# Kernel optimization log

Measured on AMD Instinct MI355X. Metric: run time of the kernel, lower is better.

Reference implementation:

```python
import jax, jax.numpy as jnp
import numpy as np

B, T, I, H, CODE = 256, 512, 1, 1024, 3


def _gru_cell(x, h, Wih, Whh, bih, bhh):
    # x: [B, I], h: [B, H]; torch nn.GRU gate math
    gi = x @ Wih.T + bih            # [B, 3H]
    gh = h @ Whh.T + bhh            # [B, 3H]
    i_r, i_z, i_n = jnp.split(gi, 3, axis=-1)
    h_r, h_z, h_n = jnp.split(gh, 3, axis=-1)
    r = jax.nn.sigmoid(i_r + h_r)
    z = jax.nn.sigmoid(i_z + h_z)
    n = jnp.tanh(i_n + r * h_n)
    return (1.0 - z) * n + z * h


def setup_inputs() -> dict:
    key = jax.random.key(0)
    ks = jax.random.split(key, 16)
    s_i = 1.0 / np.sqrt(H)
    u = lambda k, shape, s: jax.random.uniform(k, shape, jnp.float32, -s, s)
    inp = {
        "input": jax.random.normal(ks[0], (B, T, I), jnp.float32),
        "hidden_state": jnp.zeros((B, H), jnp.float32),
        # encoder GRU
        "Wih_e": u(ks[1], (3 * H, I), s_i), "Whh_e": u(ks[2], (3 * H, H), s_i),
        "bih_e": u(ks[3], (3 * H,), s_i), "bhh_e": u(ks[4], (3 * H,), s_i),
        # linear_enc: H -> 3
        "Wenc": u(ks[5], (CODE, H), s_i), "benc": u(ks[6], (CODE,), s_i),
        # linear_dec: 3 -> H
        "Wdec": u(ks[7], (H, CODE), 1.0 / np.sqrt(CODE)), "bdec": u(ks[8], (H,), 1.0 / np.sqrt(CODE)),
        # decoder GRU
        "Wih_d": u(ks[9], (3 * H, I), s_i), "Whh_d": u(ks[10], (3 * H, H), s_i),
        "bih_d": u(ks[11], (3 * H,), s_i), "bhh_d": u(ks[12], (3 * H,), s_i),
        # linear_out: H -> I
        "Wout": u(ks[13], (I, H), s_i), "bout": u(ks[14], (I,), s_i),
    }
    return inp


def reference(input, hidden_state, Wih_e, Whh_e, bih_e, bhh_e,
              Wenc, benc, Wdec, bdec, Wih_d, Whh_d, bih_d, bhh_d, Wout, bout):
    # ---- Encoder: GRU over the sequence, keep final hidden state ----
    xs = jnp.swapaxes(input, 0, 1)  # [T, B, I]

    def enc_step(h, x_t):
        h = _gru_cell(x_t, h, Wih_e, Whh_e, bih_e, bhh_e)
        return h, None

    h_T, _ = jax.lax.scan(enc_step, hidden_state, xs)
    # bottleneck: linear H->3 + sigmoid (use_linear, use_activation)
    features = jax.nn.sigmoid(h_T @ Wenc.T + benc)  # [B, 3]

    h0 = features @ Wdec.T + bdec                   # [B, H]
    x0 = jnp.zeros((input.shape[0], I), input.dtype)

    def dec_step(carry, _):
        x, h = carry
        h = _gru_cell(x, h, Wih_d, Whh_d, bih_d, bhh_d)
        x = h @ Wout.T + bout                       # [B, I]
        return (x, h), x

    _, ys = jax.lax.scan(dec_step, (x0, h0), None, length=T)  # [T, B, I]
    output = jnp.swapaxes(ys, 0, 1)                 # [B, T, I]

    # ---- Masked MSE (mask is all ones in the source -> plain mean) ----
    loss = jnp.mean((input - output) ** 2)
    return loss, features, output
```

## Files before the change

### kernel.cpp

```cpp
#include <hip/hip_runtime.h>
#include <math.h>

#define B 256
#define T 512
#define H 1024
#define CODE 3
#define NBLK 256

typedef _Float16 f16x8 __attribute__((ext_vector_type(8)));
typedef float f32x4 __attribute__((ext_vector_type(4)));

__device__ __forceinline__ float sigmoidf_(float x) { return 1.0f / (1.0f + __expf(-x)); }
__device__ __forceinline__ float tanhf_(float x) {
    float ax = fabsf(x);
    float t = __expf(-2.0f * ax);
    float r = (1.0f - t) / (1.0f + t);
    return x < 0.f ? -r : r;
}

__device__ __forceinline__ void store_f16_coh(_Float16* p, float v) {
    unsigned u = (unsigned)__builtin_bit_cast(unsigned short, (_Float16)v);
    asm volatile("global_store_short %0, %1, off sc0 sc1" :: "v"(p), "v"(u) : "memory");
}
__device__ __forceinline__ uint4 load_b16_coh(const void* p) {
    uint4 v;
    asm volatile("global_load_dwordx4 %0, %1, off sc0 sc1" : "=v"(v) : "v"(p));
    return v;
}
__device__ __forceinline__ void storef_coh(float* p, float v) {
    __hip_atomic_store(p, v, __ATOMIC_RELAXED, __HIP_MEMORY_SCOPE_AGENT);
}
__device__ __forceinline__ float loadf_coh(const float* p) {
    return __hip_atomic_load((float*)p, __ATOMIC_RELAXED, __HIP_MEMORY_SCOPE_AGENT);
}

__device__ __forceinline__ void bt_barrier(unsigned* flags, int bt, int jt,
                                           unsigned g, int tid) {
    asm volatile("s_waitcnt vmcnt(0)" ::: "memory");
    __syncthreads();
    if (tid == 0)
        __hip_atomic_store(&flags[(bt * 16 + jt) * 32], g,
                           __ATOMIC_RELAXED, __HIP_MEMORY_SCOPE_AGENT);
    if (tid < 16) {
        while (__hip_atomic_load(&flags[(bt * 16 + tid) * 32],
                                 __ATOMIC_RELAXED, __HIP_MEMORY_SCOPE_AGENT) < g)
            __builtin_amdgcn_s_sleep(1);
    }
    __syncthreads();
}

__device__ __forceinline__ void load_weights(f16x8 (&wB)[48], const float* __restrict__ W,
                                             int j, int kh, int kg) {
#pragma unroll
    for (int g = 0; g < 3; ++g)
#pragma unroll
        for (int i = 0; i < 16; ++i) {
            const float* p = W + (((size_t)g << 10) + j) * 1024 + (kh << 9) + (i << 5) + (kg << 3);
            float4 u = *(const float4*)p;
            float4 v = *(const float4*)(p + 4);
            f16x8 o;
            o[0] = (_Float16)u.x; o[1] = (_Float16)u.y; o[2] = (_Float16)u.z; o[3] = (_Float16)u.w;
            o[4] = (_Float16)v.x; o[5] = (_Float16)v.y; o[6] = (_Float16)v.z; o[7] = (_Float16)v.w;
            wB[g * 16 + i] = o;
        }
}

template <bool DEC>
__device__ __forceinline__ void phase(
    int b0, int bt, int jt, int j, int np, int kh, int kg, int r16, int tid, int lane,
    const f16x8 (&wB)[48], float (&hreg)[4],
    _Float16* __restrict__ h16A, _Float16* __restrict__ h16B,
    const float* __restrict__ Wih, const float* __restrict__ bih,
    const float* __restrict__ bhh,
    const float* __restrict__ input, const float* __restrict__ Wout, float bout_v,
    float* __restrict__ xpart, float* __restrict__ outp,
    unsigned* flags, unsigned& g,
    char* Als, f32x4 (*red)[3][64], float* xv_s, float (*xnp)[16])
{
    const float wi_r = Wih[j], wi_z = Wih[1024 + j], wi_n = Wih[2048 + j];
    const float bi_r = bih[j], bi_z = bih[1024 + j], bi_n = bih[2048 + j];
    const float bh_r = bhh[j], bh_z = bhh[1024 + j], bh_n = bhh[2048 + j];
    const float wo = DEC ? Wout[j] : 0.f;
    const int kc = tid & 127;
    const int rb = tid >> 7;

    for (int t = 0; t < T; ++t) {
        const _Float16* hp = (t & 1) ? h16B : h16A;
        _Float16* hn = (t & 1) ? h16A : h16B;

        if (DEC) {
            if (tid < 16) {
                float s = 0.f;
                if (t > 0) {
                    const float* xp = xpart + ((t - 1) & 1) * 4096 + (size_t)(b0 + tid) * 16;
#pragma unroll
                    for (int q = 0; q < 16; ++q) s += loadf_coh(xp + q);
                    s += bout_v;
                    if (jt == 0) outp[(size_t)(b0 + tid) * T + (t - 1)] = s;
                }
                xv_s[tid] = s;
            }
        }

        uint4 tmp[4];
#pragma unroll
        for (int i = 0; i < 4; ++i) {
            int row = i * 4 + rb;
            tmp[i] = load_b16_coh(hp + (((size_t)(b0 + row)) << 10) + (kc << 3));
        }
        asm volatile("s_waitcnt vmcnt(0)" ::: "memory");
#pragma unroll
        for (int i = 0; i < 4; ++i) {
            int row = i * 4 + rb;
            *(uint4*)(Als + row * 2048 + ((kc << 4) ^ ((row & 7) << 4))) = tmp[i];
        }
        __syncthreads();

        f32x4 aR = {0.f, 0.f, 0.f, 0.f}, aZ = {0.f, 0.f, 0.f, 0.f}, aN = {0.f, 0.f, 0.f, 0.f};
#pragma unroll
        for (int i = 0; i < 16; ++i) {
            int kb = (kh << 10) + (i << 6) + (kg << 4);
            f16x8 a = *(const f16x8*)(Als + (r16 << 11) + (kb ^ ((r16 & 7) << 4)));
            aR = __builtin_amdgcn_mfma_f32_16x16x32_f16(a, wB[i], aR, 0, 0, 0);
            aZ = __builtin_amdgcn_mfma_f32_16x16x32_f16(a, wB[16 + i], aZ, 0, 0, 0);
            aN = __builtin_amdgcn_mfma_f32_16x16x32_f16(a, wB[32 + i], aN, 0, 0, 0);
        }

        if (kh == 1) {
            red[np][0][lane] = aR; red[np][1][lane] = aZ; red[np][2][lane] = aN;
        }
        __syncthreads();

        if (kh == 0) {
            f32x4 rR = red[np][0][lane], rZ = red[np][1][lane], rN = red[np][2][lane];
            float xw[4];
#pragma unroll
            for (int reg = 0; reg < 4; ++reg) {
                int brow = kg * 4 + reg;
                int b = b0 + brow;
                float xv = DEC ? xv_s[brow] : input[(size_t)b * T + t];
                float r = sigmoidf_(xv * wi_r + bi_r + aR[reg] + rR[reg] + bh_r);
                float z = sigmoidf_(xv * wi_z + bi_z + aZ[reg] + rZ[reg] + bh_z);
                float n = tanhf_(xv * wi_n + bi_n + r * (aN[reg] + rN[reg] + bh_n));
                float hNew = (1.f - z) * n + z * hreg[reg];
                hreg[reg] = hNew;
                store_f16_coh(hn + ((size_t)b << 10) + j, hNew);
                xw[reg] = hNew * wo;
            }
            if (DEC) {
#pragma unroll
                for (int reg = 0; reg < 4; ++reg) {
                    float v = xw[reg];
                    v += __shfl_xor(v, 1); v += __shfl_xor(v, 2);
                    v += __shfl_xor(v, 4); v += __shfl_xor(v, 8);
                    if (r16 == 0) xnp[np][kg * 4 + reg] = v;
                }
            }
        }
        if (DEC) {
            __syncthreads();
            if (tid < 16) {
                float s = xnp[0][tid] + xnp[1][tid] + xnp[2][tid] + xnp[3][tid];
                storef_coh(xpart + (t & 1) * 4096 + (size_t)(b0 + tid) * 16 + jt, s);
            }
        }
        bt_barrier(flags, bt, jt, ++g, tid);
    }
}

__global__ __launch_bounds__(512, 2) void gru_persistent(
    const float* __restrict__ input, const float* __restrict__ h_init,
    const float* __restrict__ Wih_e, const float* __restrict__ Whh_e,
    const float* __restrict__ bih_e, const float* __restrict__ bhh_e,
    const float* __restrict__ Wenc, const float* __restrict__ benc,
    const float* __restrict__ Wdec, const float* __restrict__ bdec,
    const float* __restrict__ Wih_d, const float* __restrict__ Whh_d,
    const float* __restrict__ bih_d, const float* __restrict__ bhh_d,
    const float* __restrict__ Wout, const float* __restrict__ boutp,
    float* __restrict__ featOut, float* __restrict__ outp,
    _Float16* __restrict__ h16A, _Float16* __restrict__ h16B,
    float* __restrict__ xpart, float* __restrict__ fpart,
    unsigned* flags)
{
    __shared__ __align__(16) char Als[32768];
    __shared__ f32x4 red[4][3][64];
    __shared__ float xv_s[16];
    __shared__ float xnp[4][16];
    __shared__ float fp_np[4][16][3];
    __shared__ float feats[16][3];

    const int tid = threadIdx.x;
    const int lane = tid & 63;
    const int w = tid >> 6;
    const int kh = w & 1;
    const int np = w >> 1;
    const int kg = lane >> 4;
    const int r16 = lane & 15;
    const int bid = blockIdx.x;
    const int bt = bid & 15, jt = bid >> 4;
    const int b0 = bt * 16, j0 = jt * 64;
    const int j = j0 + np * 16 + r16;
    const float bout_v = boutp[0];
    unsigned g = 0;

    f16x8 wB[48];
    float hreg[4] = {0.f, 0.f, 0.f, 0.f};

    if (kh == 0) {
#pragma unroll
        for (int reg = 0; reg < 4; ++reg) {
            int b = b0 + kg * 4 + reg;
            float v = h_init[((size_t)b << 10) + j];
            hreg[reg] = v;
            store_f16_coh(h16A + ((size_t)b << 10) + j, v);
        }
    }
    load_weights(wB, Whh_e, j, kh, kg);
    bt_barrier(flags, bt, jt, ++g, tid);

    phase<false>(b0, bt, jt, j, np, kh, kg, r16, tid, lane, wB, hreg, h16A, h16B,
                 Wih_e, bih_e, bhh_e, input, Wout, bout_v, xpart, outp,
                 flags, g, Als, red, xv_s, xnp);

    {
        float we0 = Wenc[j], we1 = Wenc[1024 + j], we2 = Wenc[2048 + j];
        if (kh == 0) {
#pragma unroll
            for (int reg = 0; reg < 4; ++reg) {
                float h = hreg[reg];
                float p0 = h * we0, p1 = h * we1, p2 = h * we2;
#pragma unroll
                for (int m = 1; m < 16; m <<= 1) {
                    p0 += __shfl_xor(p0, m);
                    p1 += __shfl_xor(p1, m);
                    p2 += __shfl_xor(p2, m);
                }
                if (r16 == 0) {
                    fp_np[np][kg * 4 + reg][0] = p0;
                    fp_np[np][kg * 4 + reg][1] = p1;
                    fp_np[np][kg * 4 + reg][2] = p2;
                }
            }
        }
        __syncthreads();
        if (tid < 48) {
            int bi = tid / 3, c = tid % 3;
            float s = fp_np[0][bi][c] + fp_np[1][bi][c] + fp_np[2][bi][c] + fp_np[3][bi][c];
            storef_coh(fpart + (size_t)(b0 + bi) * 48 + jt * 3 + c, s);
        }
        bt_barrier(flags, bt, jt, ++g, tid);

        if (tid < 48) {
            int bi = tid / 3, c = tid % 3;
            float s = 0.f;
            const float* fp = fpart + (size_t)(b0 + bi) * 48 + c;
#pragma unroll
            for (int q = 0; q < 16; ++q) s += loadf_coh(fp + q * 3);
            float f = sigmoidf_(s + benc[c]);
            feats[bi][c] = f;
            if (jt == 0) featOut[(b0 + bi) * 3 + c] = f;
        }
        __syncthreads();

        if (kh == 0) {
#pragma unroll
            for (int reg = 0; reg < 4; ++reg) {
                int brow = kg * 4 + reg;
                int b = b0 + brow;
                float v = feats[brow][0] * Wdec[j * 3 + 0] + feats[brow][1] * Wdec[j * 3 + 1] +
                          feats[brow][2] * Wdec[j * 3 + 2] + bdec[j];
                hreg[reg] = v;
                store_f16_coh(h16A + ((size_t)b << 10) + j, v);
            }
        }
        load_weights(wB, Whh_d, j, kh, kg);
        bt_barrier(flags, bt, jt, ++g, tid);
    }

    phase<true>(b0, bt, jt, j, np, kh, kg, r16, tid, lane, wB, hreg, h16A, h16B,
                Wih_d, bih_d, bhh_d, input, Wout, bout_v, xpart, outp,
                flags, g, Als, red, xv_s, xnp);

    if (jt == 0 && tid < 16) {
        const float* xp = xpart + 4096 + (size_t)(b0 + tid) * 16;
        float s = 0.f;
#pragma unroll
        for (int q = 0; q < 16; ++q) s += loadf_coh(xp + q);
        outp[(size_t)(b0 + tid) * T + (T - 1)] = s + bout_v;
    }
}

__global__ __launch_bounds__(256) void loss_partial(
    const float* __restrict__ input, const float* __restrict__ outp,
    float* __restrict__ partial)
{
    int idx = blockIdx.x * blockDim.x + threadIdx.x;
    float s = 0.f;
    for (int i = idx; i < B * T; i += gridDim.x * blockDim.x) {
        float d = input[i] - outp[i];
        s += d * d;
    }
#pragma unroll
    for (int off = 32; off; off >>= 1) s += __shfl_down(s, off);
    __shared__ float ws[4];
    if ((threadIdx.x & 63) == 0) ws[threadIdx.x >> 6] = s;
    __syncthreads();
    if (threadIdx.x == 0) partial[blockIdx.x] = ws[0] + ws[1] + ws[2] + ws[3];
}

__global__ __launch_bounds__(256) void loss_final(
    const float* __restrict__ partial, float* __restrict__ loss)
{
    int tid = threadIdx.x;
    float s = partial[tid];
#pragma unroll
    for (int off = 32; off; off >>= 1) s += __shfl_down(s, off);
    __shared__ float ws[4];
    if ((tid & 63) == 0) ws[tid >> 6] = s;
    __syncthreads();
    if (tid == 0) loss[0] = (ws[0] + ws[1] + ws[2] + ws[3]) * (1.0f / (float)(B * T));
}

extern "C" void kernel_launch(void* const* d_in, const int* in_sizes, int n_in,
                              void* d_out, int out_size, void* d_ws, size_t ws_size,
                              hipStream_t stream) {
    const float* input = (const float*)d_in[0];
    const float* h_init = (const float*)d_in[1];
    const float* Wih_e = (const float*)d_in[2];
    const float* Whh_e = (const float*)d_in[3];
    const float* bih_e = (const float*)d_in[4];
    const float* bhh_e = (const float*)d_in[5];
    const float* Wenc  = (const float*)d_in[6];
    const float* benc  = (const float*)d_in[7];
    const float* Wdec  = (const float*)d_in[8];
    const float* bdec  = (const float*)d_in[9];
    const float* Wih_d = (const float*)d_in[10];
    const float* Whh_d = (const float*)d_in[11];
    const float* bih_d = (const float*)d_in[12];
    const float* bhh_d = (const float*)d_in[13];
    const float* Wout  = (const float*)d_in[14];
    const float* bout  = (const float*)d_in[15];
    (void)in_sizes; (void)n_in; (void)out_size; (void)ws_size;

    float* out = (float*)d_out;
    float* lossp = out;
    float* feat = out + 1;
    float* outp = out + 1 + B * CODE;

    char* ws = (char*)d_ws;
    _Float16* h16A = (_Float16*)ws;                  ws += (size_t)B * H * 2;
    _Float16* h16B = (_Float16*)ws;                  ws += (size_t)B * H * 2;
    float* xpart = (float*)ws;                       ws += 2 * 4096 * 4;
    float* fpart = (float*)ws;                       ws += (size_t)B * 48 * 4;
    float* partial = (float*)ws;                     ws += 256 * 4;
    unsigned* flags = (unsigned*)ws;                 ws += 16 * 16 * 32 * 4;

    hipMemsetAsync(flags, 0, 16 * 16 * 32 * 4, stream);

    gru_persistent<<<dim3(NBLK), dim3(512), 0, stream>>>(
        input, h_init, Wih_e, Whh_e, bih_e, bhh_e, Wenc, benc, Wdec, bdec,
        Wih_d, Whh_d, bih_d, bhh_d, Wout, bout,
        feat, outp, h16A, h16B, xpart, fpart, flags);

    loss_partial<<<256, 256, 0, stream>>>(input, outp, partial);
    loss_final<<<1, 256, 0, stream>>>(partial, lossp);
}
```

Baseline: 6.513 ms.

## Split batch tile into two half-groups with separate flags and fuse decoder output projection

Each 16-row batch tile is now processed as two 8-row halves, each with its own flag group. A block can start on one half while the other half's producers are still finishing, so inter-block synchronisation overlaps with compute. The hidden state is stored in a blocked layout so each half-tile is read contiguously. The decoder output x = h·Wout is no longer built from per-block partial sums in a separate exchange buffer; each block recomputes it directly from the shared h tile using Wout held in registers. This removes a synchronisation round per step, at the cost of two waits per step, redundant MFMA work on half-empty tiles, and extra register use.

```diff
diff --git a/kernel.cpp b/kernel.cpp
--- a/kernel.cpp
+++ b/kernel.cpp
@@ -4,7 +4,6 @@
 #define B 256
 #define T 512
 #define H 1024
-#define CODE 3
 #define NBLK 256
 
 typedef _Float16 f16x8 __attribute__((ext_vector_type(8)));
@@ -34,19 +33,18 @@
     return __hip_atomic_load((float*)p, __ATOMIC_RELAXED, __HIP_MEMORY_SCOPE_AGENT);
 }
 
-__device__ __forceinline__ void bt_barrier(unsigned* flags, int bt, int jt,
-                                           unsigned g, int tid) {
+__device__ __forceinline__ void wait_group(unsigned* fl, unsigned g, int tid) {
+    if (tid < 16) {
+        while (__hip_atomic_load(&fl[tid * 32], __ATOMIC_RELAXED, __HIP_MEMORY_SCOPE_AGENT) < g)
+            __builtin_amdgcn_s_sleep(1);
+    }
+    __syncthreads();
+}
+__device__ __forceinline__ void signal_group(unsigned* fl, int jt, unsigned g, int tid) {
     asm volatile("s_waitcnt vmcnt(0)" ::: "memory");
     __syncthreads();
     if (tid == 0)
-        __hip_atomic_store(&flags[(bt * 16 + jt) * 32], g,
-                           __ATOMIC_RELAXED, __HIP_MEMORY_SCOPE_AGENT);
-    if (tid < 16) {
-        while (__hip_atomic_load(&flags[(bt * 16 + tid) * 32],
-                                 __ATOMIC_RELAXED, __HIP_MEMORY_SCOPE_AGENT) < g)
-            __builtin_amdgcn_s_sleep(1);
-    }
-    __syncthreads();
+        __hip_atomic_store(&fl[jt * 32], g, __ATOMIC_RELAXED, __HIP_MEMORY_SCOPE_AGENT);
 }
 
 __device__ __forceinline__ void load_weights(f16x8 (&wB)[48], const float* __restrict__ W,
@@ -66,105 +64,95 @@
 }
 
 template <bool DEC>
-__device__ __forceinline__ void phase(
+__device__ __forceinline__ void run_phase(
     int b0, int bt, int jt, int j, int np, int kh, int kg, int r16, int tid, int lane,
-    const f16x8 (&wB)[48], float (&hreg)[4],
-    _Float16* __restrict__ h16A, _Float16* __restrict__ h16B,
+    int wv, int ridx,
+    const f16x8 (&wB)[48], float (&hreg)[4], const float (&wout_r)[16],
+    _Float16* __restrict__ hx,
     const float* __restrict__ Wih, const float* __restrict__ bih,
     const float* __restrict__ bhh,
-    const float* __restrict__ input, const float* __restrict__ Wout, float bout_v,
-    float* __restrict__ xpart, float* __restrict__ outp,
-    unsigned* flags, unsigned& g,
-    char* Als, f32x4 (*red)[3][64], float* xv_s, float (*xnp)[16])
+    const float* __restrict__ input, float bout_v, float* __restrict__ outp,
+    unsigned* fl0, unsigned* fl1, unsigned& g0, unsigned& g1,
+    char* Als, f32x4 (*red)[3][72], float* xv_s)
 {
-    const float wi_r = Wih[j], wi_z = Wih[1024 + j], wi_n = Wih[2048 + j];
-    const float bi_r = bih[j], bi_z = bih[1024 + j], bi_n = bih[2048 + j];
-    const float bh_r = bhh[j], bh_z = bhh[1024 + j], bh_n = bhh[2048 + j];
-    const float wo = DEC ? Wout[j] : 0.f;
-    const int kc = tid & 127;
-    const int rb = tid >> 7;
+    const float wi_r = Wih[j], wi_z = Wih[H + j], wi_n = Wih[2 * H + j];
+    const float bi_r = bih[j], bi_z = bih[H + j], bi_n = bih[2 * H + j];
+    const float bh_r = bhh[j], bh_z = bhh[H + j], bh_n = bhh[2 * H + j];
+    const int p0 = tid >> 6, w8 = tid & 63;
+    const int srl = w8 >> 3, scc = w8 & 7;
 
     for (int t = 0; t < T; ++t) {
-        const _Float16* hp = (t & 1) ? h16B : h16A;
-        _Float16* hn = (t & 1) ? h16A : h16B;
-
-        if (DEC) {
-            if (tid < 16) {
-                float s = 0.f;
-                if (t > 0) {
-                    const float* xp = xpart + ((t - 1) & 1) * 4096 + (size_t)(b0 + tid) * 16;
-#pragma unroll
-                    for (int q = 0; q < 16; ++q) s += loadf_coh(xp + q);
-                    s += bout_v;
-                    if (jt == 0) outp[(size_t)(b0 + tid) * T + (t - 1)] = s;
+        const int par_r = t & 1, par_w = (t + 1) & 1;
+#pragma unroll
+        for (int s = 0; s < 2; ++s) {
+            unsigned& g = s ? g1 : g0;
+            unsigned* fl = s ? fl1 : fl0;
+            wait_group(fl, g, tid);
+
+            const _Float16* src = hx + ((size_t)(par_r * 2 + s) * 256 + bt * 16) * 512;
+            uint4 v0 = load_b16_coh(src + (size_t)p0 * 512 + w8 * 8);
+            uint4 v1 = load_b16_coh(src + (size_t)(p0 + 8) * 512 + w8 * 8);
+            asm volatile("s_waitcnt vmcnt(0)" ::: "memory");
+            {
+                int row = s * 8 + srl;
+                int xo = (row & 7) << 4;
+                *(uint4*)(Als + row * 2048 + ((((p0) * 8 + scc) * 16) ^ xo)) = v0;
+                *(uint4*)(Als + row * 2048 + ((((p0 + 8) * 8 + scc) * 16) ^ xo)) = v1;
+            }
+            __syncthreads();
+
+            if (DEC) {
+                int arow = s * 8 + wv;
+                const char* ab = Als + arow * 2048;
+                int xo = wv << 4;
+                f16x8 a0 = *(const f16x8*)(ab + ((lane * 32) ^ xo));
+                f16x8 a1 = *(const f16x8*)(ab + (((lane * 32) + 16) ^ xo));
+                float sum = 0.f;
+#pragma unroll
+                for (int i = 0; i < 8; ++i)
+                    sum += (float)a0[i] * wout_r[i] + (float)a1[i] * wout_r[8 + i];
+#pragma unroll
+                for (int m = 1; m < 64; m <<= 1) sum += __shfl_xor(sum, m);
+                if (lane == 0) {
+                    float xv = (t > 0) ? (sum + bout_v) : 0.f;
+                    xv_s[s * 8 + wv] = xv;
+                    if (t > 0 && (jt >> 3) == s && (jt & 7) == wv)
+                        outp[(size_t)(b0 + s * 8 + wv) * T + (t - 1)] = xv;
                 }
-                xv_s[tid] = s;
-            }
-        }
-
-        uint4 tmp[4];
-#pragma unroll
-        for (int i = 0; i < 4; ++i) {
-            int row = i * 4 + rb;
-            tmp[i] = load_b16_coh(hp + (((size_t)(b0 + row)) << 10) + (kc << 3));
-        }
-        asm volatile("s_waitcnt vmcnt(0)" ::: "memory");
-#pragma unroll
-        for (int i = 0; i < 4; ++i) {
-            int row = i * 4 + rb;
-            *(uint4*)(Als + row * 2048 + ((kc << 4) ^ ((row & 7) << 4))) = tmp[i];
-        }
-        __syncthreads();
-
-        f32x4 aR = {0.f, 0.f, 0.f, 0.f}, aZ = {0.f, 0.f, 0.f, 0.f}, aN = {0.f, 0.f, 0.f, 0.f};
-#pragma unroll
-        for (int i = 0; i < 16; ++i) {
-            int kb = (kh << 10) + (i << 6) + (kg << 4);
-            f16x8 a = *(const f16x8*)(Als + (r16 << 11) + (kb ^ ((r16 & 7) << 4)));
-            aR = __builtin_amdgcn_mfma_f32_16x16x32_f16(a, wB[i], aR, 0, 0, 0);
-            aZ = __builtin_amdgcn_mfma_f32_16x16x32_f16(a, wB[16 + i], aZ, 0, 0, 0);
-            aN = __builtin_amdgcn_mfma_f32_16x16x32_f16(a, wB[32 + i], aN, 0, 0, 0);
-        }
-
-        if (kh == 1) {
-            red[np][0][lane] = aR; red[np][1][lane] = aZ; red[np][2][lane] = aN;
-        }
-        __syncthreads();
-
-        if (kh == 0) {
-            f32x4 rR = red[np][0][lane], rZ = red[np][1][lane], rN = red[np][2][lane];
-            float xw[4];
-#pragma unroll
-            for (int reg = 0; reg < 4; ++reg) {
-                int brow = kg * 4 + reg;
-                int b = b0 + brow;
-                float xv = DEC ? xv_s[brow] : input[(size_t)b * T + t];
-                float r = sigmoidf_(xv * wi_r + bi_r + aR[reg] + rR[reg] + bh_r);
-                float z = sigmoidf_(xv * wi_z + bi_z + aZ[reg] + rZ[reg] + bh_z);
-                float n = tanhf_(xv * wi_n + bi_n + r * (aN[reg] + rN[reg] + bh_n));
-                float hNew = (1.f - z) * n + z * hreg[reg];
-                hreg[reg] = hNew;
-                store_f16_coh(hn + ((size_t)b << 10) + j, hNew);
-                xw[reg] = hNew * wo;
-            }
-            if (DEC) {
+            }
+
+            f32x4 aR = {0.f, 0.f, 0.f, 0.f}, aZ = {0.f, 0.f, 0.f, 0.f}, aN = {0.f, 0.f, 0.f, 0.f};
+#pragma unroll
+            for (int i = 0; i < 16; ++i) {
+                int kb = (kh << 10) + (i << 6) + (kg << 4);
+                f16x8 a = *(const f16x8*)(Als + (r16 << 11) + (kb ^ ((r16 & 7) << 4)));
+                aR = __builtin_amdgcn_mfma_f32_16x16x32_f16(a, wB[i], aR, 0, 0, 0);
+                aZ = __builtin_amdgcn_mfma_f32_16x16x32_f16(a, wB[16 + i], aZ, 0, 0, 0);
+                aN = __builtin_amdgcn_mfma_f32_16x16x32_f16(a, wB[32 + i], aN, 0, 0, 0);
+            }
+            if (kh == 1) {
+                red[np][0][ridx] = aR; red[np][1][ridx] = aZ; red[np][2][ridx] = aN;
+            }
+            __syncthreads();
+
+            if (kh == 0 && (kg >> 1) == s) {
+                f32x4 rR = red[np][0][ridx], rZ = red[np][1][ridx], rN = red[np][2][ridx];
+                _Float16* dst = hx + ((size_t)(par_w * 2 + s) * 256 + bt * 16 + jt) * 512;
 #pragma unroll
                 for (int reg = 0; reg < 4; ++reg) {
-                    float v = xw[reg];
-                    v += __shfl_xor(v, 1); v += __shfl_xor(v, 2);
-                    v += __shfl_xor(v, 4); v += __shfl_xor(v, 8);
-                    if (r16 == 0) xnp[np][kg * 4 + reg] = v;
+                    int row = kg * 4 + reg;
+                    int b = b0 + row;
+                    float xv = DEC ? xv_s[row] : input[(size_t)b * T + t];
+                    float r = sigmoidf_(xv * wi_r + bi_r + aR[reg] + rR[reg] + bh_r);
+                    float z = sigmoidf_(xv * wi_z + bi_z + aZ[reg] + rZ[reg] + bh_z);
+                    float n = tanhf_(xv * wi_n + bi_n + r * (aN[reg] + rN[reg] + bh_n));
+                    float hNew = (1.f - z) * n + z * hreg[reg];
+                    hreg[reg] = hNew;
+                    store_f16_coh(dst + (row - s * 8) * 64 + np * 16 + r16, hNew);
                 }
             }
-        }
-        if (DEC) {
-            __syncthreads();
-            if (tid < 16) {
-                float s = xnp[0][tid] + xnp[1][tid] + xnp[2][tid] + xnp[3][tid];
-                storef_coh(xpart + (t & 1) * 4096 + (size_t)(b0 + tid) * 16 + jt, s);
-            }
-        }
-        bt_barrier(flags, bt, jt, ++g, tid);
+            signal_group(fl, jt, ++g, tid);
+        }
     }
 }
 
@@ -178,67 +166,73 @@
     const float* __restrict__ bih_d, const float* __restrict__ bhh_d,
     const float* __restrict__ Wout, const float* __restrict__ boutp,
     float* __restrict__ featOut, float* __restrict__ outp,
-    _Float16* __restrict__ h16A, _Float16* __restrict__ h16B,
-    float* __restrict__ xpart, float* __restrict__ fpart,
+    _Float16* __restrict__ hx, float* __restrict__ fpart,
     unsigned* flags)
 {
     __shared__ __align__(16) char Als[32768];
-    __shared__ f32x4 red[4][3][64];
+    __shared__ f32x4 red[4][3][72];
     __shared__ float xv_s[16];
-    __shared__ float xnp[4][16];
     __shared__ float fp_np[4][16][3];
     __shared__ float feats[16][3];
 
     const int tid = threadIdx.x;
     const int lane = tid & 63;
-    const int w = tid >> 6;
-    const int kh = w & 1;
-    const int np = w >> 1;
+    const int wv = tid >> 6;
+    const int kh = wv & 1;
+    const int np = wv >> 1;
     const int kg = lane >> 4;
     const int r16 = lane & 15;
+    const int ridx = lane + (lane >> 3);
     const int bid = blockIdx.x;
     const int bt = bid & 15, jt = bid >> 4;
     const int b0 = bt * 16, j0 = jt * 64;
     const int j = j0 + np * 16 + r16;
     const float bout_v = boutp[0];
-    unsigned g = 0;
+    unsigned* fl0 = flags + bt * 512;
+    unsigned* fl1 = flags + 8192 + bt * 512;
+    unsigned g0 = 0, g1 = 0;
 
     f16x8 wB[48];
     float hreg[4] = {0.f, 0.f, 0.f, 0.f};
+    float wout_r[16] = {};
 
     if (kh == 0) {
 #pragma unroll
         for (int reg = 0; reg < 4; ++reg) {
-            int b = b0 + kg * 4 + reg;
+            int row = kg * 4 + reg;
+            int b = b0 + row;
             float v = h_init[((size_t)b << 10) + j];
             hreg[reg] = v;
-            store_f16_coh(h16A + ((size_t)b << 10) + j, v);
+            int s = kg >> 1;
+            _Float16* dst = hx + ((size_t)(0 * 2 + s) * 256 + bt * 16 + jt) * 512;
+            store_f16_coh(dst + (row - s * 8) * 64 + np * 16 + r16, v);
         }
     }
     load_weights(wB, Whh_e, j, kh, kg);
-    bt_barrier(flags, bt, jt, ++g, tid);
-
-    phase<false>(b0, bt, jt, j, np, kh, kg, r16, tid, lane, wB, hreg, h16A, h16B,
-                 Wih_e, bih_e, bhh_e, input, Wout, bout_v, xpart, outp,
-                 flags, g, Als, red, xv_s, xnp);
+    signal_group(fl0, jt, ++g0, tid);
+    signal_group(fl1, jt, ++g1, tid);
+
+    run_phase<false>(b0, bt, jt, j, np, kh, kg, r16, tid, lane, wv, ridx,
+                     wB, hreg, wout_r, hx, Wih_e, bih_e, bhh_e,
+                     input, bout_v, outp, fl0, fl1, g0, g1, Als, red, xv_s);
 
     {
-        float we0 = Wenc[j], we1 = Wenc[1024 + j], we2 = Wenc[2048 + j];
+        float we0 = Wenc[j], we1 = Wenc[H + j], we2 = Wenc[2 * H + j];
         if (kh == 0) {
 #pragma unroll
             for (int reg = 0; reg < 4; ++reg) {
                 float h = hreg[reg];
-                float p0 = h * we0, p1 = h * we1, p2 = h * we2;
+                float q0 = h * we0, q1 = h * we1, q2 = h * we2;
 #pragma unroll
                 for (int m = 1; m < 16; m <<= 1) {
-                    p0 += __shfl_xor(p0, m);
-                    p1 += __shfl_xor(p1, m);
-                    p2 += __shfl_xor(p2, m);
+                    q0 += __shfl_xor(q0, m);
+                    q1 += __shfl_xor(q1, m);
+                    q2 += __shfl_xor(q2, m);
                 }
                 if (r16 == 0) {
-                    fp_np[np][kg * 4 + reg][0] = p0;
-                    fp_np[np][kg * 4 + reg][1] = p1;
-                    fp_np[np][kg * 4 + reg][2] = p2;
+                    fp_np[np][kg * 4 + reg][0] = q0;
+                    fp_np[np][kg * 4 + reg][1] = q1;
+                    fp_np[np][kg * 4 + reg][2] = q2;
                 }
             }
         }
@@ -248,8 +242,8 @@
             float s = fp_np[0][bi][c] + fp_np[1][bi][c] + fp_np[2][bi][c] + fp_np[3][bi][c];
             storef_coh(fpart + (size_t)(b0 + bi) * 48 + jt * 3 + c, s);
         }
-        bt_barrier(flags, bt, jt, ++g, tid);
-
+        signal_group(fl0, jt, ++g0, tid);
+        wait_group(fl0, g0, tid);
         if (tid < 48) {
             int bi = tid / 3, c = tid % 3;
             float s = 0.f;
@@ -261,32 +255,68 @@
             if (jt == 0) featOut[(b0 + bi) * 3 + c] = f;
         }
         __syncthreads();
-
         if (kh == 0) {
 #pragma unroll
             for (int reg = 0; reg < 4; ++reg) {
-                int brow = kg * 4 + reg;
-                int b = b0 + brow;
-                float v = feats[brow][0] * Wdec[j * 3 + 0] + feats[brow][1] * Wdec[j * 3 + 1] +
-                          feats[brow][2] * Wdec[j * 3 + 2] + bdec[j];
+                int row = kg * 4 + reg;
+                float v = feats[row][0] * Wdec[j * 3 + 0] + feats[row][1] * Wdec[j * 3 + 1] +
+                          feats[row][2] * Wdec[j * 3 + 2] + bdec[j];
                 hreg[reg] = v;
-                store_f16_coh(h16A + ((size_t)b << 10) + j, v);
+                int s = kg >> 1;
+                _Float16* dst = hx + ((size_t)(0 * 2 + s) * 256 + bt * 16 + jt) * 512;
+                store_f16_coh(dst + (row - s * 8) * 64 + np * 16 + r16, v);
             }
         }
         load_weights(wB, Whh_d, j, kh, kg);
-        bt_barrier(flags, bt, jt, ++g, tid);
-    }
-
-    phase<true>(b0, bt, jt, j, np, kh, kg, r16, tid, lane, wB, hreg, h16A, h16B,
-                Wih_d, bih_d, bhh_d, input, Wout, bout_v, xpart, outp,
-                flags, g, Als, red, xv_s, xnp);
-
-    if (jt == 0 && tid < 16) {
-        const float* xp = xpart + 4096 + (size_t)(b0 + tid) * 16;
-        float s = 0.f;
-#pragma unroll
-        for (int q = 0; q < 16; ++q) s += loadf_coh(xp + q);
-        outp[(size_t)(b0 + tid) * T + (T - 1)] = s + bout_v;
+#pragma unroll
+        for (int i = 0; i < 4; ++i) {
+            float4 q = *(const float4*)(Wout + lane * 16 + i * 4);
+            wout_r[i * 4 + 0] = q.x; wout_r[i * 4 + 1] = q.y;
+            wout_r[i * 4 + 2] = q.z; wout_r[i * 4 + 3] = q.w;
+        }
+        signal_group(fl0, jt, ++g0, tid);
+        signal_group(fl1, jt, ++g1, tid);
+    }
+
+    run_phase<true>(b0, bt, jt, j, np, kh, kg, r16, tid, lane, wv, ridx,
+                    wB, hreg, wout_r, hx, Wih_d, bih_d, bhh_d,
+                    input, bout_v, outp, fl0, fl1, g0, g1, Als, red, xv_s);
+
+    wait_group(fl0, g0, tid);
+    wait_group(fl1, g1, tid);
+    {
+        const int p0 = tid >> 6, w8 = tid & 63;
+        const int srl = w8 >> 3, scc = w8 & 7;
+#pragma unroll
+        for (int s = 0; s < 2; ++s) {
+            const _Float16* src = hx + ((size_t)s * 256 + bt * 16) * 512;
+            uint4 v0 = load_b16_coh(src + (size_t)p0 * 512 + w8 * 8);
+            uint4 v1 = load_b16_coh(src + (size_t)(p0 + 8) * 512 + w8 * 8);
+            asm volatile("s_waitcnt vmcnt(0)" ::: "memory");
+            int row = s * 8 + srl;
+            int xo = (row & 7) << 4;
+            *(uint4*)(Als + row * 2048 + (((p0 * 8 + scc) * 16) ^ xo)) = v0;
+            *(uint4*)(Als + row * 2048 + ((((p0 + 8) * 8 + scc) * 16) ^ xo)) = v1;
+        }
+        __syncthreads();
+#pragma unroll
+        for (int s = 0; s < 2; ++s) {
+            if ((jt >> 3) == s && (jt & 7) == wv) {
+                int arow = s * 8 + wv;
+                const char* ab = Als + arow * 2048;
+                int xo = wv << 4;
+                f16x8 a0 = *(const f16x8*)(ab + ((lane * 32) ^ xo));
+                f16x8 a1 = *(const f16x8*)(ab + (((lane * 32) + 16) ^ xo));
+                float sum = 0.f;
+#pragma unroll
+                for (int i = 0; i < 8; ++i)
+                    sum += (float)a0[i] * wout_r[i] + (float)a1[i] * wout_r[8 + i];
+#pragma unroll
+                for (int m = 1; m < 64; m <<= 1) sum += __shfl_xor(sum, m);
+                if (lane == 0)
+                    outp[(size_t)(b0 + arow) * T + (T - 1)] = sum + bout_v;
+            }
+        }
     }
 }
 
@@ -345,22 +375,20 @@
     float* out = (float*)d_out;
     float* lossp = out;
     float* feat = out + 1;
-    float* outp = out + 1 + B * CODE;
+    float* outp = out + 1 + B * 3;
 
     char* ws = (char*)d_ws;
-    _Float16* h16A = (_Float16*)ws;                  ws += (size_t)B * H * 2;
-    _Float16* h16B = (_Float16*)ws;                  ws += (size_t)B * H * 2;
-    float* xpart = (float*)ws;                       ws += 2 * 4096 * 4;
+    _Float16* hx = (_Float16*)ws;                    ws += (size_t)2 * 2 * 256 * 512 * 2;
     float* fpart = (float*)ws;                       ws += (size_t)B * 48 * 4;
     float* partial = (float*)ws;                     ws += 256 * 4;
-    unsigned* flags = (unsigned*)ws;                 ws += 16 * 16 * 32 * 4;
-
-    hipMemsetAsync(flags, 0, 16 * 16 * 32 * 4, stream);
+    unsigned* flags = (unsigned*)ws;                 ws += 2 * 16 * 16 * 32 * 4;
+
+    hipMemsetAsync(flags, 0, 2 * 16 * 16 * 32 * 4, stream);
 
     gru_persistent<<<dim3(NBLK), dim3(512), 0, stream>>>(
         input, h_init, Wih_e, Whh_e, bih_e, bhh_e, Wenc, benc, Wdec, bdec,
         Wih_d, Whh_d, bih_d, bhh_d, Wout, bout,
-        feat, outp, h16A, h16B, xpart, fpart, flags);
+        feat, outp, hx, fpart, flags);
 
     loss_partial<<<256, 256, 0, stream>>>(input, outp, partial);
     loss_final<<<1, 256, 0, stream>>>(partial, lossp);
```

Measured after the change: 13.58 ms. +108.5%, slower.

## Stage hidden state in LDS for vector stores and overlap grid-barrier polling

Applied to the files above, without the earlier changes.

Each step's new hidden values go into a shared tile first. Two threads per chunk then publish the tile to global memory with coherent 128-bit stores, replacing many scattered 2-byte stores. The inter-block barrier is restructured so one wave polls the peer tags while other threads issue the stores, and the decoder's separate block sync is folded into it. The decoder's xpart reduction loads are issued alongside the hidden-state loads so their latency overlaps. In exchange there is one extra block sync per step and a small LDS buffer, and correctness depends on the ordering of the tag store after vmcnt(0).

```diff
diff --git a/kernel.cpp b/kernel.cpp
--- a/kernel.cpp
+++ b/kernel.cpp
@@ -4,11 +4,11 @@
 #define B 256
 #define T 512
 #define H 1024
-#define CODE 3
 #define NBLK 256
 
 typedef _Float16 f16x8 __attribute__((ext_vector_type(8)));
 typedef float f32x4 __attribute__((ext_vector_type(4)));
+typedef unsigned u32x4 __attribute__((ext_vector_type(4)));
 
 __device__ __forceinline__ float sigmoidf_(float x) { return 1.0f / (1.0f + __expf(-x)); }
 __device__ __forceinline__ float tanhf_(float x) {
@@ -18,12 +18,11 @@
     return x < 0.f ? -r : r;
 }
 
-__device__ __forceinline__ void store_f16_coh(_Float16* p, float v) {
-    unsigned u = (unsigned)__builtin_bit_cast(unsigned short, (_Float16)v);
-    asm volatile("global_store_short %0, %1, off sc0 sc1" :: "v"(p), "v"(u) : "memory");
-}
-__device__ __forceinline__ uint4 load_b16_coh(const void* p) {
-    uint4 v;
+__device__ __forceinline__ void store_b128_coh(void* p, u32x4 v) {
+    asm volatile("global_store_dwordx4 %0, %1, off sc0 sc1" :: "v"(p), "v"(v) : "memory");
+}
+__device__ __forceinline__ u32x4 load_b16_coh(const void* p) {
+    u32x4 v;
     asm volatile("global_load_dwordx4 %0, %1, off sc0 sc1" : "=v"(v) : "v"(p));
     return v;
 }
@@ -32,21 +31,6 @@
 }
 __device__ __forceinline__ float loadf_coh(const float* p) {
     return __hip_atomic_load((float*)p, __ATOMIC_RELAXED, __HIP_MEMORY_SCOPE_AGENT);
-}
-
-__device__ __forceinline__ void bt_barrier(unsigned* flags, int bt, int jt,
-                                           unsigned g, int tid) {
-    asm volatile("s_waitcnt vmcnt(0)" ::: "memory");
-    __syncthreads();
-    if (tid == 0)
-        __hip_atomic_store(&flags[(bt * 16 + jt) * 32], g,
-                           __ATOMIC_RELAXED, __HIP_MEMORY_SCOPE_AGENT);
-    if (tid < 16) {
-        while (__hip_atomic_load(&flags[(bt * 16 + tid) * 32],
-                                 __ATOMIC_RELAXED, __HIP_MEMORY_SCOPE_AGENT) < g)
-            __builtin_amdgcn_s_sleep(1);
-    }
-    __syncthreads();
 }
 
 __device__ __forceinline__ void load_weights(f16x8 (&wB)[48], const float* __restrict__ W,
@@ -65,54 +49,79 @@
         }
 }
 
+#define PUBLISH_SYNC(hn_expr, EXTRA_STORES)                                              \
+    do {                                                                                 \
+        if (tid < 64) {                                                                  \
+            _Float16* hn_ = (hn_expr);                                                   \
+            int ch0 = tid, ch1 = tid + 64;                                               \
+            store_b128_coh(hn_ + ((size_t)(b0 + (ch0 >> 3)) << 10) + j0 + (ch0 & 7) * 8, \
+                           *(const u32x4*)&hout[ch0 >> 3][(ch0 & 7) * 8]);               \
+            store_b128_coh(hn_ + ((size_t)(b0 + (ch1 >> 3)) << 10) + j0 + (ch1 & 7) * 8, \
+                           *(const u32x4*)&hout[ch1 >> 3][(ch1 & 7) * 8]);               \
+        }                                                                                \
+        EXTRA_STORES                                                                     \
+        if (tid >= 128 && tid < 144) {                                                   \
+            unsigned tgt = gcur + 1;                                                     \
+            while (__hip_atomic_load(&tags[(bt * 16 + (tid - 128)) * 32],                \
+                                     __ATOMIC_RELAXED, __HIP_MEMORY_SCOPE_AGENT) < tgt)  \
+                __builtin_amdgcn_s_sleep(1);                                             \
+        }                                                                                \
+        if (tid < 64) {                                                                  \
+            asm volatile("s_waitcnt vmcnt(0)" ::: "memory");                             \
+            if (tid == 0)                                                                \
+                __hip_atomic_store(&tags[(bt * 16 + jt) * 32], gcur + 1,                 \
+                                   __ATOMIC_RELAXED, __HIP_MEMORY_SCOPE_AGENT);          \
+        }                                                                                \
+        __syncthreads();                                                                 \
+        ++gcur;                                                                          \
+    } while (0)
+
 template <bool DEC>
-__device__ __forceinline__ void phase(
-    int b0, int bt, int jt, int j, int np, int kh, int kg, int r16, int tid, int lane,
+__device__ __forceinline__ void run_phase(
+    int b0, int j0, int bt, int jt, int j, int np, int kh, int kg, int r16,
+    int tid, int lane,
     const f16x8 (&wB)[48], float (&hreg)[4],
     _Float16* __restrict__ h16A, _Float16* __restrict__ h16B,
     const float* __restrict__ Wih, const float* __restrict__ bih,
     const float* __restrict__ bhh,
     const float* __restrict__ input, const float* __restrict__ Wout, float bout_v,
     float* __restrict__ xpart, float* __restrict__ outp,
-    unsigned* flags, unsigned& g,
-    char* Als, f32x4 (*red)[3][64], float* xv_s, float (*xnp)[16])
+    unsigned* tags, unsigned& gcur,
+    char* Als, f32x4 (*red)[3][64], _Float16 (*hout)[64], float* xv_s, float (*xnp)[16])
 {
-    const float wi_r = Wih[j], wi_z = Wih[1024 + j], wi_n = Wih[2048 + j];
-    const float bi_r = bih[j], bi_z = bih[1024 + j], bi_n = bih[2048 + j];
-    const float bh_r = bhh[j], bh_z = bhh[1024 + j], bh_n = bhh[2048 + j];
+    const float wi_r = Wih[j], wi_z = Wih[H + j], wi_n = Wih[2 * H + j];
+    const float bi_r = bih[j], bi_z = bih[H + j], bi_n = bih[2 * H + j];
+    const float bh_r = bhh[j], bh_z = bhh[H + j], bh_n = bhh[2 * H + j];
     const float wo = DEC ? Wout[j] : 0.f;
-    const int kc = tid & 127;
-    const int rb = tid >> 7;
+    const int kc = tid & 127, rb = tid >> 7;
 
     for (int t = 0; t < T; ++t) {
         const _Float16* hp = (t & 1) ? h16B : h16A;
         _Float16* hn = (t & 1) ? h16A : h16B;
 
-        if (DEC) {
-            if (tid < 16) {
-                float s = 0.f;
-                if (t > 0) {
-                    const float* xp = xpart + ((t - 1) & 1) * 4096 + (size_t)(b0 + tid) * 16;
-#pragma unroll
-                    for (int q = 0; q < 16; ++q) s += loadf_coh(xp + q);
-                    s += bout_v;
-                    if (jt == 0) outp[(size_t)(b0 + tid) * T + (t - 1)] = s;
-                }
-                xv_s[tid] = s;
-            }
-        }
-
-        uint4 tmp[4];
+        u32x4 tmp[4];
 #pragma unroll
         for (int i = 0; i < 4; ++i) {
             int row = i * 4 + rb;
-            tmp[i] = load_b16_coh(hp + (((size_t)(b0 + row)) << 10) + (kc << 3));
+            tmp[i] = load_b16_coh(hp + ((size_t)(b0 + row) << 10) + (kc << 3));
+        }
+        float xg = 0.f;
+        if (DEC && t > 0 && tid < 16) {
+            const float* xp = xpart + ((t - 1) & 1) * 4096 + (size_t)(b0 + tid) * 16;
+#pragma unroll
+            for (int q = 0; q < 16; ++q) xg += loadf_coh(xp + q);
+            xg += bout_v;
         }
         asm volatile("s_waitcnt vmcnt(0)" ::: "memory");
+        if (DEC && tid < 16) {
+            float xv = (t > 0) ? xg : 0.f;
+            xv_s[tid] = xv;
+            if (t > 0 && jt == 0) outp[(size_t)(b0 + tid) * T + (t - 1)] = xv;
+        }
 #pragma unroll
         for (int i = 0; i < 4; ++i) {
             int row = i * 4 + rb;
-            *(uint4*)(Als + row * 2048 + ((kc << 4) ^ ((row & 7) << 4))) = tmp[i];
+            *(u32x4*)(Als + row * 2048 + ((kc << 4) ^ ((row & 7) << 4))) = tmp[i];
         }
         __syncthreads();
 
@@ -125,7 +134,6 @@
             aZ = __builtin_amdgcn_mfma_f32_16x16x32_f16(a, wB[16 + i], aZ, 0, 0, 0);
             aN = __builtin_amdgcn_mfma_f32_16x16x32_f16(a, wB[32 + i], aN, 0, 0, 0);
         }
-
         if (kh == 1) {
             red[np][0][lane] = aR; red[np][1][lane] = aZ; red[np][2][lane] = aN;
         }
@@ -133,38 +141,33 @@
 
         if (kh == 0) {
             f32x4 rR = red[np][0][lane], rZ = red[np][1][lane], rN = red[np][2][lane];
-            float xw[4];
 #pragma unroll
             for (int reg = 0; reg < 4; ++reg) {
-                int brow = kg * 4 + reg;
-                int b = b0 + brow;
-                float xv = DEC ? xv_s[brow] : input[(size_t)b * T + t];
+                int row = kg * 4 + reg;
+                int b = b0 + row;
+                float xv = DEC ? xv_s[row] : input[(size_t)b * T + t];
                 float r = sigmoidf_(xv * wi_r + bi_r + aR[reg] + rR[reg] + bh_r);
                 float z = sigmoidf_(xv * wi_z + bi_z + aZ[reg] + rZ[reg] + bh_z);
                 float n = tanhf_(xv * wi_n + bi_n + r * (aN[reg] + rN[reg] + bh_n));
                 float hNew = (1.f - z) * n + z * hreg[reg];
                 hreg[reg] = hNew;
-                store_f16_coh(hn + ((size_t)b << 10) + j, hNew);
-                xw[reg] = hNew * wo;
-            }
-            if (DEC) {
-#pragma unroll
-                for (int reg = 0; reg < 4; ++reg) {
-                    float v = xw[reg];
+                hout[row][np * 16 + r16] = (_Float16)hNew;
+                if (DEC) {
+                    float v = hNew * wo;
                     v += __shfl_xor(v, 1); v += __shfl_xor(v, 2);
                     v += __shfl_xor(v, 4); v += __shfl_xor(v, 8);
-                    if (r16 == 0) xnp[np][kg * 4 + reg] = v;
+                    if (r16 == 0) xnp[np][row] = v;
                 }
             }
         }
-        if (DEC) {
-            __syncthreads();
-            if (tid < 16) {
-                float s = xnp[0][tid] + xnp[1][tid] + xnp[2][tid] + xnp[3][tid];
-                storef_coh(xpart + (t & 1) * 4096 + (size_t)(b0 + tid) * 16 + jt, s);
+        __syncthreads();
+
+        PUBLISH_SYNC(hn,
+            if (DEC && tid < 16) {
+                float s_ = xnp[0][tid] + xnp[1][tid] + xnp[2][tid] + xnp[3][tid];
+                storef_coh(xpart + (t & 1) * 4096 + (size_t)(b0 + tid) * 16 + jt, s_);
             }
-        }
-        bt_barrier(flags, bt, jt, ++g, tid);
+        );
     }
 }
 
@@ -180,10 +183,11 @@
     float* __restrict__ featOut, float* __restrict__ outp,
     _Float16* __restrict__ h16A, _Float16* __restrict__ h16B,
     float* __restrict__ xpart, float* __restrict__ fpart,
-    unsigned* flags)
+    unsigned* tags)
 {
     __shared__ __align__(16) char Als[32768];
     __shared__ f32x4 red[4][3][64];
+    __shared__ __align__(16) _Float16 hout[16][64];
     __shared__ float xv_s[16];
     __shared__ float xnp[4][16];
     __shared__ float fp_np[4][16][3];
@@ -191,9 +195,9 @@
 
     const int tid = threadIdx.x;
     const int lane = tid & 63;
-    const int w = tid >> 6;
-    const int kh = w & 1;
-    const int np = w >> 1;
+    const int wv = tid >> 6;
+    const int kh = wv & 1;
+    const int np = wv >> 1;
     const int kg = lane >> 4;
     const int r16 = lane & 15;
     const int bid = blockIdx.x;
@@ -201,7 +205,7 @@
     const int b0 = bt * 16, j0 = jt * 64;
     const int j = j0 + np * 16 + r16;
     const float bout_v = boutp[0];
-    unsigned g = 0;
+    unsigned gcur = 0;
 
     f16x8 wB[48];
     float hreg[4] = {0.f, 0.f, 0.f, 0.f};
@@ -209,36 +213,37 @@
     if (kh == 0) {
 #pragma unroll
         for (int reg = 0; reg < 4; ++reg) {
-            int b = b0 + kg * 4 + reg;
-            float v = h_init[((size_t)b << 10) + j];
+            int row = kg * 4 + reg;
+            float v = h_init[((size_t)(b0 + row) << 10) + j];
             hreg[reg] = v;
-            store_f16_coh(h16A + ((size_t)b << 10) + j, v);
-        }
-    }
+            hout[row][np * 16 + r16] = (_Float16)v;
+        }
+    }
+    __syncthreads();
+    PUBLISH_SYNC(h16A, );
     load_weights(wB, Whh_e, j, kh, kg);
-    bt_barrier(flags, bt, jt, ++g, tid);
-
-    phase<false>(b0, bt, jt, j, np, kh, kg, r16, tid, lane, wB, hreg, h16A, h16B,
-                 Wih_e, bih_e, bhh_e, input, Wout, bout_v, xpart, outp,
-                 flags, g, Als, red, xv_s, xnp);
+
+    run_phase<false>(b0, j0, bt, jt, j, np, kh, kg, r16, tid, lane, wB, hreg,
+                     h16A, h16B, Wih_e, bih_e, bhh_e, input, Wout, bout_v,
+                     xpart, outp, tags, gcur, Als, red, hout, xv_s, xnp);
 
     {
-        float we0 = Wenc[j], we1 = Wenc[1024 + j], we2 = Wenc[2048 + j];
+        float we0 = Wenc[j], we1 = Wenc[H + j], we2 = Wenc[2 * H + j];
         if (kh == 0) {
 #pragma unroll
             for (int reg = 0; reg < 4; ++reg) {
                 float h = hreg[reg];
-                float p0 = h * we0, p1 = h * we1, p2 = h * we2;
+                float q0 = h * we0, q1 = h * we1, q2 = h * we2;
 #pragma unroll
                 for (int m = 1; m < 16; m <<= 1) {
-                    p0 += __shfl_xor(p0, m);
-                    p1 += __shfl_xor(p1, m);
-                    p2 += __shfl_xor(p2, m);
+                    q0 += __shfl_xor(q0, m);
+                    q1 += __shfl_xor(q1, m);
+                    q2 += __shfl_xor(q2, m);
                 }
                 if (r16 == 0) {
-                    fp_np[np][kg * 4 + reg][0] = p0;
-                    fp_np[np][kg * 4 + reg][1] = p1;
-                    fp_np[np][kg * 4 + reg][2] = p2;
+                    fp_np[np][kg * 4 + reg][0] = q0;
+                    fp_np[np][kg * 4 + reg][1] = q1;
+                    fp_np[np][kg * 4 + reg][2] = q2;
                 }
             }
         }
@@ -248,7 +253,20 @@
             float s = fp_np[0][bi][c] + fp_np[1][bi][c] + fp_np[2][bi][c] + fp_np[3][bi][c];
             storef_coh(fpart + (size_t)(b0 + bi) * 48 + jt * 3 + c, s);
         }
-        bt_barrier(flags, bt, jt, ++g, tid);
+        if (tid >= 128 && tid < 144) {
+            unsigned tgt = gcur + 1;
+            while (__hip_atomic_load(&tags[(bt * 16 + (tid - 128)) * 32],
+                                     __ATOMIC_RELAXED, __HIP_MEMORY_SCOPE_AGENT) < tgt)
+                __builtin_amdgcn_s_sleep(1);
+        }
+        if (tid < 64) {
+            asm volatile("s_waitcnt vmcnt(0)" ::: "memory");
+            if (tid == 0)
+                __hip_atomic_store(&tags[(bt * 16 + jt) * 32], gcur + 1,
+                                   __ATOMIC_RELAXED, __HIP_MEMORY_SCOPE_AGENT);
+        }
+        __syncthreads();
+        ++gcur;
 
         if (tid < 48) {
             int bi = tid / 3, c = tid % 3;
@@ -265,21 +283,21 @@
         if (kh == 0) {
 #pragma unroll
             for (int reg = 0; reg < 4; ++reg) {
-                int brow = kg * 4 + reg;
-                int b = b0 + brow;
-                float v = feats[brow][0] * Wdec[j * 3 + 0] + feats[brow][1] * Wdec[j * 3 + 1] +
-                          feats[brow][2] * Wdec[j * 3 + 2] + bdec[j];
+                int row = kg * 4 + reg;
+                float v = feats[row][0] * Wdec[j * 3 + 0] + feats[row][1] * Wdec[j * 3 + 1] +
+                          feats[row][2] * Wdec[j * 3 + 2] + bdec[j];
                 hreg[reg] = v;
-                store_f16_coh(h16A + ((size_t)b << 10) + j, v);
+                hout[row][np * 16 + r16] = (_Float16)v;
             }
         }
+        __syncthreads();
+        PUBLISH_SYNC(h16A, );
         load_weights(wB, Whh_d, j, kh, kg);
-        bt_barrier(flags, bt, jt, ++g, tid);
-    }
-
-    phase<true>(b0, bt, jt, j, np, kh, kg, r16, tid, lane, wB, hreg, h16A, h16B,
-                Wih_d, bih_d, bhh_d, input, Wout, bout_v, xpart, outp,
-                flags, g, Als, red, xv_s, xnp);
+    }
+
+    run_phase<true>(b0, j0, bt, jt, j, np, kh, kg, r16, tid, lane, wB, hreg,
+                    h16A, h16B, Wih_d, bih_d, bhh_d, input, Wout, bout_v,
+                    xpart, outp, tags, gcur, Als, red, hout, xv_s, xnp);
 
     if (jt == 0 && tid < 16) {
         const float* xp = xpart + 4096 + (size_t)(b0 + tid) * 16;
@@ -345,7 +363,7 @@
     float* out = (float*)d_out;
     float* lossp = out;
     float* feat = out + 1;
-    float* outp = out + 1 + B * CODE;
+    float* outp = out + 1 + B * 3;
 
     char* ws = (char*)d_ws;
     _Float16* h16A = (_Float16*)ws;                  ws += (size_t)B * H * 2;
@@ -353,14 +371,14 @@
     float* xpart = (float*)ws;                       ws += 2 * 4096 * 4;
     float* fpart = (float*)ws;                       ws += (size_t)B * 48 * 4;
     float* partial = (float*)ws;                     ws += 256 * 4;
-    unsigned* flags = (unsigned*)ws;                 ws += 16 * 16 * 32 * 4;
-
-    hipMemsetAsync(flags, 0, 16 * 16 * 32 * 4, stream);
+    unsigned* tags = (unsigned*)ws;                  ws += 16 * 16 * 32 * 4;
+
+    hipMemsetAsync(tags, 0, 16 * 16 * 32 * 4, stream);
 
     gru_persistent<<<dim3(NBLK), dim3(512), 0, stream>>>(
         input, h_init, Wih_e, Whh_e, bih_e, bhh_e, Wenc, benc, Wdec, bdec,
         Wih_d, Whh_d, bih_d, bhh_d, Wout, bout,
-        feat, outp, h16A, h16B, xpart, fpart, flags);
+        feat, outp, h16A, h16B, xpart, fpart, tags);
 
     loss_partial<<<256, 256, 0, stream>>>(input, outp, partial);
     loss_final<<<1, 256, 0, stream>>>(partial, lossp);
```

Measured after the change: 5.966 ms (median of 3 runs). -8.4%, faster.
